# Kernel tuning notes

Hardware: AMD Instinct MI355X
Metric: run time of the kernel (lower is better)

The kernel has to match this reference:

```python
import jax, jax.numpy as jnp
import numpy as np

B, I, H = 8192, 1024, 1024

def setup_inputs() -> dict:
    key = jax.random.key(0)
    ks = jax.random.split(key, 5)
    # xavier-uniform-ish scale for weights
    sW = float(np.sqrt(6.0 / (I + H)))
    sU = float(np.sqrt(6.0 / (H + H)))
    return {
        "x": jax.random.normal(ks[0], (B, I), jnp.float32),
        "h": jax.random.normal(ks[1], (B, H), jnp.float32),
        "c": jax.random.normal(ks[2], (B, H), jnp.float32),
        # gate order along leading axis: 0=i, 1=f, 2=o, 3=c_hat
        "W": jax.random.uniform(ks[3], (4, H, I), jnp.float32, -sW, sW),
        "bW": jnp.zeros((4, H), jnp.float32),
        "U": jax.random.uniform(ks[4], (4, H, H), jnp.float32, -sU, sU),
        "bU": jnp.zeros((4, H), jnp.float32),
    }

def reference(x, h, c, W, bW, U, bU):
    # two batched GEMMs covering all 8 original Linear layers
    gx = jnp.einsum('bi,ghi->gbh', x, W) + bW[:, None, :]   # [4,B,H]
    gh = jnp.einsum('bk,ghk->gbh', h, U) + bU[:, None, :]   # [4,B,H]
    g = gx + gh
    i = jax.nn.sigmoid(g[0])
    f = jax.nn.sigmoid(g[1])
    o = jax.nn.sigmoid(g[2])
    c_hat = jnp.tanh(g[3])
    c_new = f * c + i * c_hat
    h_new = o * jnp.tanh(c_new)
    return (h_new, (h_new, c_new))
```

## Files before the change

kernel.cpp:

```cpp
#include <hip/hip_runtime.h>
#include <hip/hip_bf16.h>

typedef __hip_bfloat16 bf16;
typedef __attribute__((ext_vector_type(8))) short short8;
typedef __attribute__((ext_vector_type(4))) float floatx4;

#define B_DIM 8192
#define H_DIM 1024
#define KSUM 2048
#define BM 128
#define BN 128
#define BK 32
#define CEX_STRIDE 68

union BS { bf16 b; short s; };
__device__ __forceinline__ short cvt1(float f) {
  BS u; u.b = __float2bfloat16(f); return u.s;
}
__device__ __forceinline__ short8 cvt8(float4 lo, float4 hi) {
  short8 r;
  r[0] = cvt1(lo.x); r[1] = cvt1(lo.y); r[2] = cvt1(lo.z); r[3] = cvt1(lo.w);
  r[4] = cvt1(hi.x); r[5] = cvt1(hi.y); r[6] = cvt1(hi.z); r[7] = cvt1(hi.w);
  return r;
}

__device__ __forceinline__ void async_ld16(const bf16* g, bf16* lds) {
  __builtin_amdgcn_global_load_lds(
      (const __attribute__((address_space(1))) unsigned int*)g,
      (__attribute__((address_space(3))) unsigned int*)lds,
      16, 0, 0);
}

__global__ __launch_bounds__(256) void cvt_pack_A(
    const float* __restrict__ x, const float* __restrict__ h,
    bf16* __restrict__ Ac) {
  const int idx = blockIdx.x * 256 + threadIdx.x;
  const long row = idx >> 8;
  const int k0 = (idx & 255) << 3;
  const float* src = (k0 < 1024) ? (x + row * 1024 + k0)
                                 : (h + row * 1024 + (k0 - 1024));
  const float4 lo = *(const float4*)src;
  const float4 hi = *(const float4*)(src + 4);
  *(short8*)(Ac + row * KSUM + k0) = cvt8(lo, hi);
}

__global__ __launch_bounds__(256) void cvt_pack_B(
    const float* __restrict__ W, const float* __restrict__ U,
    bf16* __restrict__ Bc) {
  const int idx = blockIdx.x * 256 + threadIdx.x;
  const long r = idx >> 8;
  const int k0 = (idx & 255) << 3;
  const int g = (int)(r & 3);
  const long hh = r >> 2;
  const long base = (long)g * (H_DIM * H_DIM) + hh * H_DIM;
  const float* src = (k0 < 1024) ? (W + base + k0) : (U + base + (k0 - 1024));
  const float4 lo = *(const float4*)src;
  const float4 hi = *(const float4*)(src + 4);
  *(short8*)(Bc + r * KSUM + k0) = cvt8(lo, hi);
}

__device__ __forceinline__ float sigmoidf_(float v) {
  return 1.0f / (1.0f + __expf(-v));
}
__device__ __forceinline__ float tanhf_(float v) {
  return 1.0f - 2.0f / (__expf(2.0f * v) + 1.0f);
}
__device__ __forceinline__ float getc(const float4& v, int t) {
  return t == 0 ? v.x : t == 1 ? v.y : t == 2 ? v.z : v.w;
}

__global__ __launch_bounds__(256) void gemm_lstm(
    const bf16* __restrict__ Ac, const bf16* __restrict__ Bc,
    const float* __restrict__ cprev_g, const float* __restrict__ bW,
    const float* __restrict__ bU, float* __restrict__ out) {
  __shared__ __align__(16) char smem[4 * 16 * CEX_STRIDE * 4];
  bf16* sA = (bf16*)smem;
  bf16* sB = (bf16*)(smem + 8192);
  float* cex = (float*)smem;

  const int tid  = threadIdx.x;
  const int lane = tid & 63;
  const int wv   = tid >> 6;

  const int nt = blockIdx.x & 31;
  const int mt = blockIdx.x >> 5;
  const long m0 = (long)mt * BM;
  const long n0 = (long)nt * BN;

  const int sr  = (wv << 4) + (lane >> 2);
  const int skk = (lane & 3) << 3;
  const bf16* aG = Ac + (m0 + sr) * (long)KSUM + skk;
  const bf16* bG = Bc + (n0 + sr) * (long)KSUM + skk;
  bf16* sA0 = sA + (wv << 9);
  bf16* sA1 = sA + (wv << 9) + 2048;
  bf16* sB0 = sB + (wv << 9);
  bf16* sB1 = sB + (wv << 9) + 2048;

  const int wm = ((wv >> 1) & 1) << 6;
  const int wn = (wv & 1) << 6;
  const int col16 = lane & 15;
  const int fk = (lane >> 4) << 3;

  floatx4 acc[4][4];
#pragma unroll
  for (int i = 0; i < 4; ++i)
#pragma unroll
    for (int j = 0; j < 4; ++j) acc[i][j] = (floatx4){0.f, 0.f, 0.f, 0.f};

  for (int kt = 0; kt < 64; ++kt) {
    const long koff = (long)kt * BK;
    __syncthreads();
    async_ld16(aG + koff, sA0);
    async_ld16(aG + 64 * (long)KSUM + koff, sA1);
    async_ld16(bG + koff, sB0);
    async_ld16(bG + 64 * (long)KSUM + koff, sB1);
    __syncthreads();

    short8 af[4], bfr[4];
#pragma unroll
    for (int i = 0; i < 4; ++i) {
      af[i]  = *(const short8*)&sA[(wm + i * 16 + col16) * BK + fk];
      bfr[i] = *(const short8*)&sB[(wn + i * 16 + col16) * BK + fk];
    }
#pragma unroll
    for (int i = 0; i < 4; ++i)
#pragma unroll
      for (int j = 0; j < 4; ++j)
        acc[i][j] = __builtin_amdgcn_mfma_f32_16x16x32_bf16(af[i], bfr[j],
                                                            acc[i][j], 0, 0, 0);
  }

  __syncthreads();

  const int rquad = (lane >> 4) << 2;
  const int row16 = lane & 15;
  const int tq    = lane >> 4;
  const long hglob = (n0 >> 2) + (wn >> 2) + tq * 4;

  float4 bsum[4];
#pragma unroll
  for (int g = 0; g < 4; ++g) {
    const float4 a = *(const float4*)(bW + g * H_DIM + hglob);
    const float4 b = *(const float4*)(bU + g * H_DIM + hglob);
    bsum[g] = (float4){a.x + b.x, a.y + b.y, a.z + b.z, a.w + b.w};
  }

  float* wx = cex + wv * (16 * CEX_STRIDE);
  const long BH = (long)B_DIM * H_DIM;

  for (int ig = 0; ig < 4; ++ig) {
#pragma unroll
    for (int j = 0; j < 4; ++j)
#pragma unroll
      for (int r = 0; r < 4; ++r)
        wx[(rquad + r) * CEX_STRIDE + j * 16 + col16] = acc[ig][j][r];

    float4 g4[4];
#pragma unroll
    for (int t = 0; t < 4; ++t)
      g4[t] = *(const float4*)&wx[row16 * CEX_STRIDE + (tq * 4 + t) * 4];

    const long mrow = m0 + wm + ig * 16 + row16;
    const float4 cp = *(const float4*)(cprev_g + mrow * H_DIM + hglob);

    float hn[4], cn[4];
#pragma unroll
    for (int t = 0; t < 4; ++t) {
      const float gi = g4[t].x + getc(bsum[0], t);
      const float gf = g4[t].y + getc(bsum[1], t);
      const float go = g4[t].z + getc(bsum[2], t);
      const float gg = g4[t].w + getc(bsum[3], t);
      const float I = sigmoidf_(gi);
      const float F = sigmoidf_(gf);
      const float O = sigmoidf_(go);
      const float G = tanhf_(gg);
      const float cv = F * getc(cp, t) + I * G;
      hn[t] = O * tanhf_(cv);
      cn[t] = cv;
    }
    const float4 hn4 = {hn[0], hn[1], hn[2], hn[3]};
    const float4 cn4 = {cn[0], cn[1], cn[2], cn[3]};
    const long ob = mrow * H_DIM + hglob;
    *(float4*)(out + ob)          = hn4;
    *(float4*)(out + BH + ob)     = hn4;
    *(float4*)(out + 2 * BH + ob) = cn4;
  }
}

extern "C" void kernel_launch(void* const* d_in, const int* in_sizes, int n_in,
                              void* d_out, int out_size, void* d_ws, size_t ws_size,
                              hipStream_t stream) {
  const float* x  = (const float*)d_in[0];
  const float* h  = (const float*)d_in[1];
  const float* c  = (const float*)d_in[2];
  const float* W  = (const float*)d_in[3];
  const float* bW = (const float*)d_in[4];
  const float* U  = (const float*)d_in[5];
  const float* bU = (const float*)d_in[6];
  float* out = (float*)d_out;

  bf16* Ac = (bf16*)d_ws;
  bf16* Bc = (bf16*)((char*)d_ws + (size_t)33554432);

  cvt_pack_A<<<8192, 256, 0, stream>>>(x, h, Ac);
  cvt_pack_B<<<4096, 256, 0, stream>>>(W, U, Bc);
  gemm_lstm<<<2048, 256, 0, stream>>>(Ac, Bc, c, bW, bU, out);
}
```

Before: 411.1 us.

## Double K-tile depth, XOR-swizzle LDS layout, and remap blocks per XCD

```diff
diff --git a/kernel.cpp b/kernel.cpp
--- a/kernel.cpp
+++ b/kernel.cpp
@@ -10,7 +10,8 @@
 #define KSUM 2048
 #define BM 128
 #define BN 128
-#define BK 32
+#define BK 64
+#define KITER 32
 #define CEX_STRIDE 68
 
 union BS { bf16 b; short s; };
@@ -73,33 +74,36 @@
     const bf16* __restrict__ Ac, const bf16* __restrict__ Bc,
     const float* __restrict__ cprev_g, const float* __restrict__ bW,
     const float* __restrict__ bU, float* __restrict__ out) {
-  __shared__ __align__(16) char smem[4 * 16 * CEX_STRIDE * 4];
+  __shared__ __align__(16) char smem[32768];
   bf16* sA = (bf16*)smem;
-  bf16* sB = (bf16*)(smem + 8192);
+  bf16* sB = (bf16*)(smem + 16384);
   float* cex = (float*)smem;
 
   const int tid  = threadIdx.x;
   const int lane = tid & 63;
   const int wv   = tid >> 6;
 
-  const int nt = blockIdx.x & 31;
-  const int mt = blockIdx.x >> 5;
+  const int blk  = blockIdx.x;
+  const int xcd  = blk & 7;
+  const int slot = blk >> 3;
+  const int mt   = slot & 63;
+  const int nt   = (xcd << 2) | (slot >> 6);
   const long m0 = (long)mt * BM;
   const long n0 = (long)nt * BN;
 
-  const int sr  = (wv << 4) + (lane >> 2);
-  const int skk = (lane & 3) << 3;
-  const bf16* aG = Ac + (m0 + sr) * (long)KSUM + skk;
-  const bf16* bG = Bc + (n0 + sr) * (long)KSUM + skk;
-  bf16* sA0 = sA + (wv << 9);
-  bf16* sA1 = sA + (wv << 9) + 2048;
-  bf16* sB0 = sB + (wv << 9);
-  bf16* sB1 = sB + (wv << 9) + 2048;
+  const int lrow   = lane >> 3;
+  const int lchunk = lane & 7;
+  const int schunk = lchunk ^ lrow;
+  const bf16* aSrc = Ac + (m0 + wv * 8 + lrow) * (long)KSUM + schunk * 8;
+  const bf16* bSrc = Bc + (n0 + wv * 8 + lrow) * (long)KSUM + schunk * 8;
+  bf16* sAw = sA + (wv * 8) * 64;
+  bf16* sBw = sB + (wv * 8) * 64;
 
   const int wm = ((wv >> 1) & 1) << 6;
   const int wn = (wv & 1) << 6;
   const int col16 = lane & 15;
-  const int fk = (lane >> 4) << 3;
+  const int quad  = lane >> 4;
+  const int x7    = col16 & 7;
 
   floatx4 acc[4][4];
 #pragma unroll
@@ -107,27 +111,32 @@
 #pragma unroll
     for (int j = 0; j < 4; ++j) acc[i][j] = (floatx4){0.f, 0.f, 0.f, 0.f};
 
-  for (int kt = 0; kt < 64; ++kt) {
+  for (int kt = 0; kt < KITER; ++kt) {
     const long koff = (long)kt * BK;
     __syncthreads();
-    async_ld16(aG + koff, sA0);
-    async_ld16(aG + 64 * (long)KSUM + koff, sA1);
-    async_ld16(bG + koff, sB0);
-    async_ld16(bG + 64 * (long)KSUM + koff, sB1);
+#pragma unroll
+    for (int q = 0; q < 4; ++q) {
+      async_ld16(aSrc + koff + (long)q * (32 * (long)KSUM), sAw + q * (32 * 64));
+      async_ld16(bSrc + koff + (long)q * (32 * (long)KSUM), sBw + q * (32 * 64));
+    }
     __syncthreads();
 
-    short8 af[4], bfr[4];
-#pragma unroll
-    for (int i = 0; i < 4; ++i) {
-      af[i]  = *(const short8*)&sA[(wm + i * 16 + col16) * BK + fk];
-      bfr[i] = *(const short8*)&sB[(wn + i * 16 + col16) * BK + fk];
+#pragma unroll
+    for (int s = 0; s < 2; ++s) {
+      const int cp = ((((s << 2) + quad) ^ x7) << 3);
+      short8 af[4], bfr[4];
+#pragma unroll
+      for (int i = 0; i < 4; ++i) {
+        af[i]  = *(const short8*)&sA[(wm + i * 16 + col16) * 64 + cp];
+        bfr[i] = *(const short8*)&sB[(wn + i * 16 + col16) * 64 + cp];
+      }
+#pragma unroll
+      for (int i = 0; i < 4; ++i)
+#pragma unroll
+        for (int j = 0; j < 4; ++j)
+          acc[i][j] = __builtin_amdgcn_mfma_f32_16x16x32_bf16(af[i], bfr[j],
+                                                              acc[i][j], 0, 0, 0);
     }
-#pragma unroll
-    for (int i = 0; i < 4; ++i)
-#pragma unroll
-      for (int j = 0; j < 4; ++j)
-        acc[i][j] = __builtin_amdgcn_mfma_f32_16x16x32_bf16(af[i], bfr[j],
-                                                            acc[i][j], 0, 0, 0);
   }
 
   __syncthreads();
@@ -161,7 +170,7 @@
       g4[t] = *(const float4*)&wx[row16 * CEX_STRIDE + (tq * 4 + t) * 4];
 
     const long mrow = m0 + wm + ig * 16 + row16;
-    const float4 cp = *(const float4*)(cprev_g + mrow * H_DIM + hglob);
+    const float4 cp4 = *(const float4*)(cprev_g + mrow * H_DIM + hglob);
 
     float hn[4], cn[4];
 #pragma unroll
@@ -174,7 +183,7 @@
       const float F = sigmoidf_(gf);
       const float O = sigmoidf_(go);
       const float G = tanhf_(gg);
-      const float cv = F * getc(cp, t) + I * G;
+      const float cv = F * getc(cp4, t) + I * G;
       hn[t] = O * tanhf_(cv);
       cn[t] = cv;
     }
```

Result: faster. 394.2 us (-4.1%).
